# Optimization experiments

Measured on AMD Instinct MI355X. Metric: run time of the kernel, lower is better.

## Reference

```python
import jax, jax.numpy as jnp
import numpy as np

N_NODES = 131072
N_EDGES = 4194304
H1, H2 = 16, 1


def setup_inputs() -> dict:
    key = jax.random.key(0)
    k = jax.random.split(key, 6)
    x = jax.random.uniform(k[0], (N_NODES, 2), dtype=jnp.float32)
    edge_index = jax.random.randint(k[1], (2, N_EDGES), 0, N_NODES, dtype=jnp.int64)
    # GCNConv weights (glorot-ish scale) and zero biases
    W1 = jax.random.normal(k[2], (2, H1), dtype=jnp.float32) * 0.5
    b1 = jnp.zeros((H1,), dtype=jnp.float32)
    W2 = jax.random.normal(k[3], (H1, H2), dtype=jnp.float32) * 0.25
    b2 = jnp.zeros((H2,), dtype=jnp.float32)
    return {"x": x, "W1": W1, "b1": b1, "W2": W2, "b2": b2, "edge_index": edge_index}


def gcn_layer(x, W, b, src, dst, n):
    # PyG GCNConv: h = D^{-1/2} (A+I) D^{-1/2} (x W) + b  (self-loops already in src/dst)
    h = x @ W                                              # [N, F_out]
    deg = jax.ops.segment_sum(jnp.ones(dst.shape[0], h.dtype), dst, num_segments=n)
    dinv = jax.lax.rsqrt(deg)                              # deg >= 1 thanks to self-loops
    norm = dinv[src] * dinv[dst]                           # [E+N]
    out = jax.ops.segment_sum(h[src] * norm[:, None], dst, num_segments=n)
    return out + b


def reference(x, W1, b1, W2, b2, edge_index):
    n = x.shape[0]
    loops = jnp.arange(n, dtype=edge_index.dtype)
    src = jnp.concatenate([edge_index[0], loops])          # add self-loops once
    dst = jnp.concatenate([edge_index[1], loops])
    h = jax.nn.relu(gcn_layer(x, W1, b1, src, dst, n))
    h = gcn_layer(h, W2, b2, src, dst, n)                  # [N, 1]
    scores = jax.nn.sigmoid(h)
    return scores[edge_index[0]]                           # gather per-edge source score [E, 1]
```

## Files before the change

kernel.cpp:

```cpp
#include <hip/hip_runtime.h>
#include <cmath>

typedef unsigned int uint;

constexpr int N  = 131072;
constexpr int E  = 4194304;
constexpr int F  = 16;
constexpr int NB = 512;
constexpr int NBLK  = 512;
constexpr int SCT   = 512;
constexpr int GT    = 1024;
constexpr int CHUNK = 8192;
constexpr int EPT   = 16;
constexpr int CAPB  = 9216;
constexpr int LT    = 1024;
constexpr uint SENT = 0xFFFFFFFFu;

constexpr float S1 = 4194304.0f;
constexpr float S2 = 65536.0f;

__global__ void __launch_bounds__(SCT) k_scatter(
        const int* __restrict__ src, const int* __restrict__ dst,
        uint* __restrict__ part, uint* __restrict__ dirw) {
    __shared__ uint h[NB];
    __shared__ uint wsum[8];
    __shared__ uint vals[CHUNK];
    int t = threadIdx.x, g = blockIdx.x;
    int lane = t & 63, w = t >> 6;
    h[t] = 0;
    __syncthreads();
    int d[EPT], s[EPT];
    const int4* src4 = (const int4*)src;
    const int4* dst4 = (const int4*)dst;
    int base4 = g * (CHUNK / 4);
#pragma unroll
    for (int k = 0; k < EPT / 4; ++k) {
        int4 d4 = dst4[base4 + k * SCT + t];
        int4 s4 = src4[base4 + k * SCT + t];
        d[4 * k + 0] = d4.x; d[4 * k + 1] = d4.y; d[4 * k + 2] = d4.z; d[4 * k + 3] = d4.w;
        s[4 * k + 0] = s4.x; s[4 * k + 1] = s4.y; s[4 * k + 2] = s4.z; s[4 * k + 3] = s4.w;
        atomicAdd(&h[d4.x >> 8], 1u);
        atomicAdd(&h[d4.y >> 8], 1u);
        atomicAdd(&h[d4.z >> 8], 1u);
        atomicAdd(&h[d4.w >> 8], 1u);
    }
    __syncthreads();
    uint v = h[t];
    uint sv = v;
#pragma unroll
    for (int off = 1; off < 64; off <<= 1) {
        uint n = __shfl_up(sv, off);
        if (lane >= off) sv += n;
    }
    if (lane == 63) wsum[w] = sv;
    __syncthreads();
    uint wo = 0;
    for (int i = 0; i < w; ++i) wo += wsum[i];
    sv += wo;
    uint ex = sv - v;
    dirw[(size_t)g * NB + t] = v | (ex << 16);
    __syncthreads();
    h[t] = ex;
    __syncthreads();
#pragma unroll
    for (int k = 0; k < EPT; ++k) {
        int b = d[k] >> 8;
        uint slot = atomicAdd(&h[b], 1u);
        vals[slot] = ((uint)s[k] << 8) | (uint)(d[k] & 255);
    }
    __syncthreads();
    uint4* part4 = (uint4*)(part + (size_t)g * CHUNK);
    const uint4* vals4 = (const uint4*)vals;
#pragma unroll
    for (int k = 0; k < EPT / 4; ++k)
        part4[k * SCT + t] = vals4[k * SCT + t];
}

__global__ void __launch_bounds__(GT) k_gather(
        const uint* __restrict__ part, const uint* __restrict__ dirw,
        const float* __restrict__ x,
        uint* __restrict__ part2, uint* __restrict__ blen,
        float* __restrict__ dinv, float2* __restrict__ y) {
    __shared__ uint ps[NB + 1];
    __shared__ uint segoff[NB];
    __shared__ uint hw[16 * 256];
    __shared__ uint wsum[8];
    int t = threadIdx.x, b = blockIdx.x;
    int lane = t & 63, w = t >> 6;
#pragma unroll
    for (int k = 0; k < 4; ++k) hw[k * GT + t] = 0;
    if (t < NB) {
        uint pd = dirw[(size_t)t * NB + b];
        uint len = pd & 0xFFFFu;
        segoff[t] = (uint)t * CHUNK + (pd >> 16);
        uint sv = len;
#pragma unroll
        for (int off = 1; off < 64; off <<= 1) {
            uint n = __shfl_up(sv, off);
            if (lane >= off) sv += n;
        }
        if (lane == 63) wsum[w] = sv;
        ps[t] = sv - len;
    }
    __syncthreads();
    if (t < NB) {
        uint wo = 0;
        for (int i = 0; i < w; ++i) wo += wsum[i];
        ps[t] += wo;
    }
    if (t == 0) {
        uint Lt = 0;
#pragma unroll
        for (int i = 0; i < 8; ++i) Lt += wsum[i];
        ps[NB] = Lt;
    }
    __syncthreads();
    uint L = ps[NB];
    uint* o2 = part2 + (size_t)b * CAPB;
    int sub = lane >> 4, l16 = lane & 15;
#pragma unroll
    for (int pass = 0; pass < 8; ++pass) {
        int r = pass * 64 + w * 4 + sub;
        uint off = segoff[r], base = ps[r], len = ps[r + 1] - base;
        for (uint j = l16; j < len; j += 16) {
            uint pk = part[off + j];
            atomicAdd(&hw[w * 256 + (pk & 255u)], 1u);
            if (base + j < (uint)CAPB) o2[base + j] = pk;
        }
    }
    __syncthreads();
    uint Lc = (L > (uint)CAPB) ? (uint)CAPB : L;
    uint Lp = (Lc + 3u) & ~3u;
    uint i2 = Lc + (uint)t;
    if (i2 < Lp) o2[i2] = SENT;
    if (t == 0) blen[b] = Lp;
    if (t < 256) {
        uint c = 0;
#pragma unroll
        for (int k = 0; k < 16; ++k) c += hw[k * 256 + t];
        int node = (b << 8) + t;
        float di = rsqrtf(1.0f + (float)c);
        dinv[node] = di;
        float2 xv = ((const float2*)x)[node];
        y[node] = make_float2(di * xv.x, di * xv.y);
    }
}

__global__ void __launch_bounds__(LT) k_l1(
        const uint* __restrict__ part2, const uint* __restrict__ blen,
        const float2* __restrict__ y, const float* __restrict__ dinv,
        const float* __restrict__ W1, const float* __restrict__ b1,
        const float* __restrict__ W2, float* __restrict__ g2) {
    __shared__ int a0[16 * 256], a1[16 * 256];
    int t = threadIdx.x, b = blockIdx.x, w = t >> 6;
#pragma unroll
    for (int k = 0; k < 4; ++k) { a0[k * LT + t] = 0; a1[k * LT + t] = 0; }
    __syncthreads();
    uint L4 = blen[b] >> 2;
    const uint4* p4 = (const uint4*)(part2 + (size_t)b * CAPB);
    for (uint i = t; i < L4; i += LT) {
        uint4 q = p4[i];
        bool v0 = q.x != SENT, v1 = q.y != SENT, v2 = q.z != SENT, v3 = q.w != SENT;
        float2 y0, y1, y2, y3;
        if (v0) y0 = y[q.x >> 8];
        if (v1) y1 = y[q.y >> 8];
        if (v2) y2 = y[q.z >> 8];
        if (v3) y3 = y[q.w >> 8];
        if (v0) { atomicAdd(&a0[w * 256 + (q.x & 255u)], __float2int_rn(y0.x * S1));
                  atomicAdd(&a1[w * 256 + (q.x & 255u)], __float2int_rn(y0.y * S1)); }
        if (v1) { atomicAdd(&a0[w * 256 + (q.y & 255u)], __float2int_rn(y1.x * S1));
                  atomicAdd(&a1[w * 256 + (q.y & 255u)], __float2int_rn(y1.y * S1)); }
        if (v2) { atomicAdd(&a0[w * 256 + (q.z & 255u)], __float2int_rn(y2.x * S1));
                  atomicAdd(&a1[w * 256 + (q.z & 255u)], __float2int_rn(y2.y * S1)); }
        if (v3) { atomicAdd(&a0[w * 256 + (q.w & 255u)], __float2int_rn(y3.x * S1));
                  atomicAdd(&a1[w * 256 + (q.w & 255u)], __float2int_rn(y3.y * S1)); }
    }
    __syncthreads();
    if (t < 256) {
        int s0 = 0, s1 = 0;
#pragma unroll
        for (int k = 0; k < 16; ++k) { s0 += a0[k * 256 + t]; s1 += a1[k * 256 + t]; }
        int node = (b << 8) + t;
        float di = dinv[node];
        float2 yn = y[node];
        float A0 = di * ((float)s0 * (1.0f / S1) + yn.x);
        float A1 = di * ((float)s1 * (1.0f / S1) + yn.y);
        float acc = 0.0f;
#pragma unroll
        for (int f = 0; f < F; ++f) {
            float v = fmaf(A0, W1[f], fmaf(A1, W1[F + f], b1[f]));
            acc = fmaf(fmaxf(v, 0.0f), W2[f], acc);
        }
        g2[node] = di * acc;
    }
}

__global__ void __launch_bounds__(LT) k_l2(
        const uint* __restrict__ part2, const uint* __restrict__ blen,
        const float* __restrict__ g2, const float* __restrict__ dinv,
        const float* __restrict__ b2, float* __restrict__ scores) {
    __shared__ int a[16 * 256];
    int t = threadIdx.x, b = blockIdx.x, w = t >> 6;
#pragma unroll
    for (int k = 0; k < 4; ++k) a[k * LT + t] = 0;
    __syncthreads();
    uint L4 = blen[b] >> 2;
    const uint4* p4 = (const uint4*)(part2 + (size_t)b * CAPB);
    for (uint i = t; i < L4; i += LT) {
        uint4 q = p4[i];
        uint pk;
#pragma unroll
        for (int k = 0; k < 4; ++k) {
            pk = (k == 0) ? q.x : (k == 1) ? q.y : (k == 2) ? q.z : q.w;
            if (pk != SENT)
                atomicAdd(&a[w * 256 + (pk & 255u)], __float2int_rn(g2[pk >> 8] * S2));
        }
    }
    __syncthreads();
    if (t < 256) {
        int s = 0;
#pragma unroll
        for (int k = 0; k < 16; ++k) s += a[k * 256 + t];
        int node = (b << 8) + t;
        float acc = (float)s * (1.0f / S2);
        float v = fmaf(dinv[node], acc + g2[node], b2[0]);
        scores[node] = 1.0f / (1.0f + expf(-v));
    }
}

__global__ void k_out(const int* __restrict__ src, const float* __restrict__ scores,
                      float* __restrict__ out) {
    int i = blockIdx.x * blockDim.x + threadIdx.x;
    if (i >= E / 4) return;
    int4 s4 = ((const int4*)src)[i];
    float4 o;
    o.x = scores[s4.x];
    o.y = scores[s4.y];
    o.z = scores[s4.z];
    o.w = scores[s4.w];
    ((float4*)out)[i] = o;
}

extern "C" void kernel_launch(void* const* d_in, const int* in_sizes, int n_in,
                              void* d_out, int out_size, void* d_ws, size_t ws_size,
                              hipStream_t stream) {
    const float* x  = (const float*)d_in[0];
    const float* W1 = (const float*)d_in[1];
    const float* b1 = (const float*)d_in[2];
    const float* W2 = (const float*)d_in[3];
    const float* b2 = (const float*)d_in[4];
    const int*   ei = (const int*)d_in[5];
    const int* src = ei;
    const int* dst = ei + E;

    uint* dirw    = (uint*)d_ws;
    uint* blen    = dirw + (size_t)NBLK * NB;
    float* dinv   = (float*)(blen + NB);
    float2* y     = (float2*)(dinv + N);
    float* g2     = (float*)(y + N);
    float* scores = g2 + N;
    uint* part2   = (uint*)(scores + N);

    uint* part  = (uint*)d_out;
    float* out  = (float*)d_out;

    k_scatter<<<NBLK,        SCT, 0, stream>>>(src, dst, part, dirw);
    k_gather <<<NB,          GT,  0, stream>>>(part, dirw, x, part2, blen, dinv, y);
    k_l1     <<<NB,          LT,  0, stream>>>(part2, blen, y, dinv, W1, b1, W2, g2);
    k_l2     <<<NB,          LT,  0, stream>>>(part2, blen, g2, dinv, b2, scores);
    k_out    <<<E / 4 / 256, 256, 0, stream>>>(src, scores, out);
}
```

Baseline: 164.8 us.

## Fuse all stages into one persistent kernel with grid-wide barriers

Merges the scatter, gather, two aggregation layers and output gather into a single persistent kernel of 512 blocks. The stages are separated by software grid barriers built on global atomics. Each block keeps its destination-bucket edge list in shared memory (the old part2 staging buffer), along with its dinv, y and g2 values, which removes global round-trips and several launch overheads. The barrier requires all 512 blocks to be co-resident; if they are not, the timeout guard lets blocks run ahead and read incomplete data. Block size also drops from 1024 to 512 threads in the aggregation stages.

```diff
diff --git a/kernel.cpp b/kernel.cpp
--- a/kernel.cpp
+++ b/kernel.cpp
@@ -7,90 +7,123 @@
 constexpr int E  = 4194304;
 constexpr int F  = 16;
 constexpr int NB = 512;
-constexpr int NBLK  = 512;
-constexpr int SCT   = 512;
-constexpr int GT    = 1024;
+constexpr int T  = 512;
 constexpr int CHUNK = 8192;
 constexpr int EPT   = 16;
 constexpr int CAPB  = 9216;
-constexpr int LT    = 1024;
 constexpr uint SENT = 0xFFFFFFFFu;
 
 constexpr float S1 = 4194304.0f;
 constexpr float S2 = 65536.0f;
 
-__global__ void __launch_bounds__(SCT) k_scatter(
+__device__ __forceinline__ void gsync(uint* cnt, uint* rel, int t, uint gen) {
+    __syncthreads();
+    if (t == 0) {
+        __threadfence();
+        uint v = __hip_atomic_fetch_add(cnt, 1u, __ATOMIC_ACQ_REL,
+                                        __HIP_MEMORY_SCOPE_AGENT);
+        if (v == (uint)(NB - 1)) {
+            __hip_atomic_store(cnt, 0u, __ATOMIC_RELAXED, __HIP_MEMORY_SCOPE_AGENT);
+            __hip_atomic_store(rel, gen, __ATOMIC_RELEASE, __HIP_MEMORY_SCOPE_AGENT);
+        } else {
+            int guard = 0;
+            while (__hip_atomic_load(rel, __ATOMIC_ACQUIRE,
+                                     __HIP_MEMORY_SCOPE_AGENT) < gen) {
+                __builtin_amdgcn_s_sleep(2);
+                if (++guard > (1 << 22)) break;
+            }
+        }
+        __threadfence();
+    }
+    __syncthreads();
+}
+
+__global__ void k_init(uint* bar) {
+    if (threadIdx.x < 64) bar[threadIdx.x] = 0;
+}
+
+__global__ void __launch_bounds__(T, 4) k_fused(
         const int* __restrict__ src, const int* __restrict__ dst,
-        uint* __restrict__ part, uint* __restrict__ dirw) {
-    __shared__ uint h[NB];
+        const float* __restrict__ x,
+        const float* __restrict__ W1, const float* __restrict__ b1,
+        const float* __restrict__ W2, const float* __restrict__ b2,
+        uint* __restrict__ dirw, float2* __restrict__ y,
+        float* __restrict__ g2, float* __restrict__ scores,
+        uint* bar,
+        uint* part_out ) {
+    __shared__ uint stage[CAPB];
+    __shared__ uint ps[NB + 1];
+    __shared__ uint segoff[NB];
+    __shared__ int  bins0[8 * 256];
+    __shared__ int  bins1[8 * 256];
+    __shared__ float  dl[256];
+    __shared__ float2 yl[256];
+    __shared__ float  g2l[256];
     __shared__ uint wsum[8];
-    __shared__ uint vals[CHUNK];
+
     int t = threadIdx.x, g = blockIdx.x;
     int lane = t & 63, w = t >> 6;
-    h[t] = 0;
+    uint* part = part_out;
+    uint* cnt = bar;
+    uint* rel = bar + 32;
+
+    ps[t] = 0;
     __syncthreads();
     int d[EPT], s[EPT];
-    const int4* src4 = (const int4*)src;
-    const int4* dst4 = (const int4*)dst;
-    int base4 = g * (CHUNK / 4);
-#pragma unroll
-    for (int k = 0; k < EPT / 4; ++k) {
-        int4 d4 = dst4[base4 + k * SCT + t];
-        int4 s4 = src4[base4 + k * SCT + t];
-        d[4 * k + 0] = d4.x; d[4 * k + 1] = d4.y; d[4 * k + 2] = d4.z; d[4 * k + 3] = d4.w;
-        s[4 * k + 0] = s4.x; s[4 * k + 1] = s4.y; s[4 * k + 2] = s4.z; s[4 * k + 3] = s4.w;
-        atomicAdd(&h[d4.x >> 8], 1u);
-        atomicAdd(&h[d4.y >> 8], 1u);
-        atomicAdd(&h[d4.z >> 8], 1u);
-        atomicAdd(&h[d4.w >> 8], 1u);
-    }
-    __syncthreads();
-    uint v = h[t];
-    uint sv = v;
-#pragma unroll
-    for (int off = 1; off < 64; off <<= 1) {
-        uint n = __shfl_up(sv, off);
-        if (lane >= off) sv += n;
-    }
-    if (lane == 63) wsum[w] = sv;
-    __syncthreads();
-    uint wo = 0;
-    for (int i = 0; i < w; ++i) wo += wsum[i];
-    sv += wo;
-    uint ex = sv - v;
-    dirw[(size_t)g * NB + t] = v | (ex << 16);
-    __syncthreads();
-    h[t] = ex;
-    __syncthreads();
-#pragma unroll
-    for (int k = 0; k < EPT; ++k) {
-        int b = d[k] >> 8;
-        uint slot = atomicAdd(&h[b], 1u);
-        vals[slot] = ((uint)s[k] << 8) | (uint)(d[k] & 255);
-    }
-    __syncthreads();
-    uint4* part4 = (uint4*)(part + (size_t)g * CHUNK);
-    const uint4* vals4 = (const uint4*)vals;
-#pragma unroll
-    for (int k = 0; k < EPT / 4; ++k)
-        part4[k * SCT + t] = vals4[k * SCT + t];
-}
-
-__global__ void __launch_bounds__(GT) k_gather(
-        const uint* __restrict__ part, const uint* __restrict__ dirw,
-        const float* __restrict__ x,
-        uint* __restrict__ part2, uint* __restrict__ blen,
-        float* __restrict__ dinv, float2* __restrict__ y) {
-    __shared__ uint ps[NB + 1];
-    __shared__ uint segoff[NB];
-    __shared__ uint hw[16 * 256];
-    __shared__ uint wsum[8];
-    int t = threadIdx.x, b = blockIdx.x;
-    int lane = t & 63, w = t >> 6;
-#pragma unroll
-    for (int k = 0; k < 4; ++k) hw[k * GT + t] = 0;
-    if (t < NB) {
-        uint pd = dirw[(size_t)t * NB + b];
+    {
+        const int4* src4 = (const int4*)src;
+        const int4* dst4 = (const int4*)dst;
+        int base4 = g * (CHUNK / 4);
+#pragma unroll
+        for (int k = 0; k < EPT / 4; ++k) {
+            int4 d4 = dst4[base4 + k * T + t];
+            int4 s4 = src4[base4 + k * T + t];
+            d[4 * k + 0] = d4.x; d[4 * k + 1] = d4.y; d[4 * k + 2] = d4.z; d[4 * k + 3] = d4.w;
+            s[4 * k + 0] = s4.x; s[4 * k + 1] = s4.y; s[4 * k + 2] = s4.z; s[4 * k + 3] = s4.w;
+            atomicAdd(&ps[d4.x >> 8], 1u);
+            atomicAdd(&ps[d4.y >> 8], 1u);
+            atomicAdd(&ps[d4.z >> 8], 1u);
+            atomicAdd(&ps[d4.w >> 8], 1u);
+        }
+    }
+    __syncthreads();
+    {
+        uint v = ps[t];
+        uint sv = v;
+#pragma unroll
+        for (int off = 1; off < 64; off <<= 1) {
+            uint n = __shfl_up(sv, off);
+            if (lane >= off) sv += n;
+        }
+        if (lane == 63) wsum[w] = sv;
+        __syncthreads();
+        uint wo = 0;
+        for (int i = 0; i < w; ++i) wo += wsum[i];
+        sv += wo;
+        uint ex = sv - v;
+        dirw[(size_t)g * NB + t] = v | (ex << 16);
+        __syncthreads();
+        ps[t] = ex;
+        __syncthreads();
+#pragma unroll
+        for (int k = 0; k < EPT; ++k) {
+            int b = d[k] >> 8;
+            uint slot = atomicAdd(&ps[b], 1u);
+            stage[slot] = ((uint)s[k] << 8) | (uint)(d[k] & 255);
+        }
+        __syncthreads();
+        uint4* part4 = (uint4*)(part + (size_t)g * CHUNK);
+        const uint4* st4 = (const uint4*)stage;
+#pragma unroll
+        for (int k = 0; k < EPT / 4; ++k)
+            part4[k * T + t] = st4[k * T + t];
+    }
+    gsync(cnt, rel, t, 1);
+
+#pragma unroll
+    for (int k = 0; k < 4; ++k) bins0[k * T + t] = 0;
+    {
+        uint pd = dirw[(size_t)t * NB + g];
         uint len = pd & 0xFFFFu;
         segoff[t] = (uint)t * CHUNK + (pd >> 16);
         uint sv = len;
@@ -100,89 +133,84 @@
             if (lane >= off) sv += n;
         }
         if (lane == 63) wsum[w] = sv;
-        ps[t] = sv - len;
-    }
-    __syncthreads();
-    if (t < NB) {
+        uint part_ps = sv - len;
+        __syncthreads();
         uint wo = 0;
         for (int i = 0; i < w; ++i) wo += wsum[i];
-        ps[t] += wo;
-    }
-    if (t == 0) {
-        uint Lt = 0;
-#pragma unroll
-        for (int i = 0; i < 8; ++i) Lt += wsum[i];
-        ps[NB] = Lt;
-    }
-    __syncthreads();
-    uint L = ps[NB];
-    uint* o2 = part2 + (size_t)b * CAPB;
-    int sub = lane >> 4, l16 = lane & 15;
-#pragma unroll
-    for (int pass = 0; pass < 8; ++pass) {
-        int r = pass * 64 + w * 4 + sub;
-        uint off = segoff[r], base = ps[r], len = ps[r + 1] - base;
-        for (uint j = l16; j < len; j += 16) {
-            uint pk = part[off + j];
-            atomicAdd(&hw[w * 256 + (pk & 255u)], 1u);
-            if (base + j < (uint)CAPB) o2[base + j] = pk;
-        }
-    }
-    __syncthreads();
+        ps[t] = part_ps + wo;
+        if (t == 0) {
+            uint Lt = 0;
+#pragma unroll
+            for (int i = 0; i < 8; ++i) Lt += wsum[i];
+            ps[NB] = Lt;
+        }
+    }
+    __syncthreads();
+    uint L  = ps[NB];
     uint Lc = (L > (uint)CAPB) ? (uint)CAPB : L;
     uint Lp = (Lc + 3u) & ~3u;
-    uint i2 = Lc + (uint)t;
-    if (i2 < Lp) o2[i2] = SENT;
-    if (t == 0) blen[b] = Lp;
+    {
+        int sub = lane >> 4, l16 = lane & 15;
+#pragma unroll 2
+        for (int pass = 0; pass < 16; ++pass) {
+            int r = pass * 32 + w * 4 + sub;
+            uint off = segoff[r], base = ps[r], len = ps[r + 1] - base;
+            for (uint j = l16; j < len; j += 16) {
+                uint pk = part[off + j];
+                atomicAdd((uint*)&bins0[w * 256 + (pk & 255u)], 1u);
+                if (base + j < (uint)CAPB) stage[base + j] = pk;
+            }
+        }
+        uint i2 = Lc + (uint)t;
+        if (i2 < Lp) stage[i2] = SENT;
+    }
+    __syncthreads();
     if (t < 256) {
         uint c = 0;
 #pragma unroll
-        for (int k = 0; k < 16; ++k) c += hw[k * 256 + t];
-        int node = (b << 8) + t;
+        for (int k = 0; k < 8; ++k) c += (uint)bins0[k * 256 + t];
+        int node = (g << 8) + t;
         float di = rsqrtf(1.0f + (float)c);
-        dinv[node] = di;
+        dl[t] = di;
         float2 xv = ((const float2*)x)[node];
-        y[node] = make_float2(di * xv.x, di * xv.y);
-    }
-}
-
-__global__ void __launch_bounds__(LT) k_l1(
-        const uint* __restrict__ part2, const uint* __restrict__ blen,
-        const float2* __restrict__ y, const float* __restrict__ dinv,
-        const float* __restrict__ W1, const float* __restrict__ b1,
-        const float* __restrict__ W2, float* __restrict__ g2) {
-    __shared__ int a0[16 * 256], a1[16 * 256];
-    int t = threadIdx.x, b = blockIdx.x, w = t >> 6;
-#pragma unroll
-    for (int k = 0; k < 4; ++k) { a0[k * LT + t] = 0; a1[k * LT + t] = 0; }
-    __syncthreads();
-    uint L4 = blen[b] >> 2;
-    const uint4* p4 = (const uint4*)(part2 + (size_t)b * CAPB);
-    for (uint i = t; i < L4; i += LT) {
-        uint4 q = p4[i];
-        bool v0 = q.x != SENT, v1 = q.y != SENT, v2 = q.z != SENT, v3 = q.w != SENT;
-        float2 y0, y1, y2, y3;
-        if (v0) y0 = y[q.x >> 8];
-        if (v1) y1 = y[q.y >> 8];
-        if (v2) y2 = y[q.z >> 8];
-        if (v3) y3 = y[q.w >> 8];
-        if (v0) { atomicAdd(&a0[w * 256 + (q.x & 255u)], __float2int_rn(y0.x * S1));
-                  atomicAdd(&a1[w * 256 + (q.x & 255u)], __float2int_rn(y0.y * S1)); }
-        if (v1) { atomicAdd(&a0[w * 256 + (q.y & 255u)], __float2int_rn(y1.x * S1));
-                  atomicAdd(&a1[w * 256 + (q.y & 255u)], __float2int_rn(y1.y * S1)); }
-        if (v2) { atomicAdd(&a0[w * 256 + (q.z & 255u)], __float2int_rn(y2.x * S1));
-                  atomicAdd(&a1[w * 256 + (q.z & 255u)], __float2int_rn(y2.y * S1)); }
-        if (v3) { atomicAdd(&a0[w * 256 + (q.w & 255u)], __float2int_rn(y3.x * S1));
-                  atomicAdd(&a1[w * 256 + (q.w & 255u)], __float2int_rn(y3.y * S1)); }
+        float2 yv = make_float2(di * xv.x, di * xv.y);
+        yl[t] = yv;
+        y[node] = yv;
+    }
+    gsync(cnt, rel, t, 2);
+
+#pragma unroll
+    for (int k = 0; k < 4; ++k) { bins0[k * T + t] = 0; bins1[k * T + t] = 0; }
+    __syncthreads();
+    uint L4 = Lp >> 2;
+    {
+        const uint4* st4 = (const uint4*)stage;
+        for (uint i = t; i < L4; i += T) {
+            uint4 q = st4[i];
+            bool v0 = q.x != SENT, v1 = q.y != SENT, v2 = q.z != SENT, v3 = q.w != SENT;
+            float2 y0, y1, y2, y3;
+            if (v0) y0 = y[q.x >> 8];
+            if (v1) y1 = y[q.y >> 8];
+            if (v2) y2 = y[q.z >> 8];
+            if (v3) y3 = y[q.w >> 8];
+            if (v0) { atomicAdd(&bins0[w * 256 + (q.x & 255u)], __float2int_rn(y0.x * S1));
+                      atomicAdd(&bins1[w * 256 + (q.x & 255u)], __float2int_rn(y0.y * S1)); }
+            if (v1) { atomicAdd(&bins0[w * 256 + (q.y & 255u)], __float2int_rn(y1.x * S1));
+                      atomicAdd(&bins1[w * 256 + (q.y & 255u)], __float2int_rn(y1.y * S1)); }
+            if (v2) { atomicAdd(&bins0[w * 256 + (q.z & 255u)], __float2int_rn(y2.x * S1));
+                      atomicAdd(&bins1[w * 256 + (q.z & 255u)], __float2int_rn(y2.y * S1)); }
+            if (v3) { atomicAdd(&bins0[w * 256 + (q.w & 255u)], __float2int_rn(y3.x * S1));
+                      atomicAdd(&bins1[w * 256 + (q.w & 255u)], __float2int_rn(y3.y * S1)); }
+        }
     }
     __syncthreads();
     if (t < 256) {
         int s0 = 0, s1 = 0;
 #pragma unroll
-        for (int k = 0; k < 16; ++k) { s0 += a0[k * 256 + t]; s1 += a1[k * 256 + t]; }
-        int node = (b << 8) + t;
-        float di = dinv[node];
-        float2 yn = y[node];
+        for (int k = 0; k < 8; ++k) { s0 += bins0[k * 256 + t]; s1 += bins1[k * 256 + t]; }
+        int node = (g << 8) + t;
+        float di = dl[t];
+        float2 yn = yl[t];
         float A0 = di * ((float)s0 * (1.0f / S1) + yn.x);
         float A1 = di * ((float)s1 * (1.0f / S1) + yn.y);
         float acc = 0.0f;
@@ -191,54 +219,54 @@
             float v = fmaf(A0, W1[f], fmaf(A1, W1[F + f], b1[f]));
             acc = fmaf(fmaxf(v, 0.0f), W2[f], acc);
         }
-        g2[node] = di * acc;
-    }
-}
-
-__global__ void __launch_bounds__(LT) k_l2(
-        const uint* __restrict__ part2, const uint* __restrict__ blen,
-        const float* __restrict__ g2, const float* __restrict__ dinv,
-        const float* __restrict__ b2, float* __restrict__ scores) {
-    __shared__ int a[16 * 256];
-    int t = threadIdx.x, b = blockIdx.x, w = t >> 6;
-#pragma unroll
-    for (int k = 0; k < 4; ++k) a[k * LT + t] = 0;
-    __syncthreads();
-    uint L4 = blen[b] >> 2;
-    const uint4* p4 = (const uint4*)(part2 + (size_t)b * CAPB);
-    for (uint i = t; i < L4; i += LT) {
-        uint4 q = p4[i];
-        uint pk;
-#pragma unroll
-        for (int k = 0; k < 4; ++k) {
-            pk = (k == 0) ? q.x : (k == 1) ? q.y : (k == 2) ? q.z : q.w;
-            if (pk != SENT)
-                atomicAdd(&a[w * 256 + (pk & 255u)], __float2int_rn(g2[pk >> 8] * S2));
+        float gg = di * acc;
+        g2l[t] = gg;
+        g2[node] = gg;
+    }
+    gsync(cnt, rel, t, 3);
+
+#pragma unroll
+    for (int k = 0; k < 4; ++k) bins0[k * T + t] = 0;
+    __syncthreads();
+    {
+        uint L4b = Lp >> 2;
+        const uint4* st4 = (const uint4*)stage;
+        for (uint i = t; i < L4b; i += T) {
+            uint4 q = st4[i];
+            uint pk;
+#pragma unroll
+            for (int k = 0; k < 4; ++k) {
+                pk = (k == 0) ? q.x : (k == 1) ? q.y : (k == 2) ? q.z : q.w;
+                if (pk != SENT)
+                    atomicAdd(&bins0[w * 256 + (pk & 255u)], __float2int_rn(g2[pk >> 8] * S2));
+            }
         }
     }
     __syncthreads();
     if (t < 256) {
-        int s = 0;
-#pragma unroll
-        for (int k = 0; k < 16; ++k) s += a[k * 256 + t];
-        int node = (b << 8) + t;
-        float acc = (float)s * (1.0f / S2);
-        float v = fmaf(dinv[node], acc + g2[node], b2[0]);
+        int sacc = 0;
+#pragma unroll
+        for (int k = 0; k < 8; ++k) sacc += bins0[k * 256 + t];
+        int node = (g << 8) + t;
+        float acc = (float)sacc * (1.0f / S2);
+        float v = fmaf(dl[t], acc + g2l[t], b2[0]);
         scores[node] = 1.0f / (1.0f + expf(-v));
     }
-}
-
-__global__ void k_out(const int* __restrict__ src, const float* __restrict__ scores,
-                      float* __restrict__ out) {
-    int i = blockIdx.x * blockDim.x + threadIdx.x;
-    if (i >= E / 4) return;
-    int4 s4 = ((const int4*)src)[i];
-    float4 o;
-    o.x = scores[s4.x];
-    o.y = scores[s4.y];
-    o.z = scores[s4.z];
-    o.w = scores[s4.w];
-    ((float4*)out)[i] = o;
+    gsync(cnt, rel, t, 4);
+
+    {
+        const int4* s4p = (const int4*)src;
+        float4* o4 = (float4*)part_out;
+        for (int i = g * T + t; i < E / 4; i += NB * T) {
+            int4 s4 = s4p[i];
+            float4 o;
+            o.x = scores[s4.x];
+            o.y = scores[s4.y];
+            o.z = scores[s4.z];
+            o.w = scores[s4.w];
+            o4[i] = o;
+        }
+    }
 }
 
 extern "C" void kernel_launch(void* const* d_in, const int* in_sizes, int n_in,
@@ -253,20 +281,14 @@
     const int* src = ei;
     const int* dst = ei + E;
 
-    uint* dirw    = (uint*)d_ws;
-    uint* blen    = dirw + (size_t)NBLK * NB;
-    float* dinv   = (float*)(blen + NB);
-    float2* y     = (float2*)(dinv + N);
-    float* g2     = (float*)(y + N);
-    float* scores = g2 + N;
-    uint* part2   = (uint*)(scores + N);
-
-    uint* part  = (uint*)d_out;
-    float* out  = (float*)d_out;
-
-    k_scatter<<<NBLK,        SCT, 0, stream>>>(src, dst, part, dirw);
-    k_gather <<<NB,          GT,  0, stream>>>(part, dirw, x, part2, blen, dinv, y);
-    k_l1     <<<NB,          LT,  0, stream>>>(part2, blen, y, dinv, W1, b1, W2, g2);
-    k_l2     <<<NB,          LT,  0, stream>>>(part2, blen, g2, dinv, b2, scores);
-    k_out    <<<E / 4 / 256, 256, 0, stream>>>(src, scores, out);
-}
+    uint*   dirw   = (uint*)d_ws;
+    float2* y      = (float2*)(dirw + (size_t)NB * NB);
+    float*  g2     = (float*)(y + N);
+    float*  scores = g2 + N;
+    uint*   bar    = (uint*)(scores + N);
+    uint*   part_out = (uint*)d_out;
+
+    k_init <<<1, 64, 0, stream>>>(bar);
+    k_fused<<<NB, T, 0, stream>>>(src, dst, x, W1, b1, W2, b2,
+                                  dirw, y, g2, scores, bar, part_out);
+}
```

Measured after the change: 352.3 us. 114% more time.

## Scatter edges directly into per-bucket lists via global atomic offsets

Applied to the files above, without the earlier changes.

The scatter kernel now reserves space in each destination bucket with a global atomicAdd on per-bucket counters and writes its locally sorted edges straight into the final bucket lists. This removes the intermediate partition buffer and the separate gather pass that re-read and recopied it, leaving a lighter kernel that only counts degrees and pads the buckets. It also software-prefetches the next uint4 in the two aggregation loops. The trade-off is nondeterministic edge order within buckets, which adds float-to-int quantisation order effects, plus an extra init launch and scattered 16-lane global writes.

```diff
diff --git a/kernel.cpp b/kernel.cpp
--- a/kernel.cpp
+++ b/kernel.cpp
@@ -9,7 +9,6 @@
 constexpr int NB = 512;
 constexpr int NBLK  = 512;
 constexpr int SCT   = 512;
-constexpr int GT    = 1024;
 constexpr int CHUNK = 8192;
 constexpr int EPT   = 16;
 constexpr int CAPB  = 9216;
@@ -19,15 +18,20 @@
 constexpr float S1 = 4194304.0f;
 constexpr float S2 = 65536.0f;
 
+__global__ void k_init(uint* gcnt) {
+    gcnt[threadIdx.x] = 0;
+}
+
 __global__ void __launch_bounds__(SCT) k_scatter(
         const int* __restrict__ src, const int* __restrict__ dst,
-        uint* __restrict__ part, uint* __restrict__ dirw) {
-    __shared__ uint h[NB];
+        uint* __restrict__ gcnt, uint* __restrict__ part2) {
+    __shared__ uint ps[NB];
+    __shared__ uint gbase[NB];
+    __shared__ uint vals[CHUNK];
     __shared__ uint wsum[8];
-    __shared__ uint vals[CHUNK];
     int t = threadIdx.x, g = blockIdx.x;
     int lane = t & 63, w = t >> 6;
-    h[t] = 0;
+    ps[t] = 0;
     __syncthreads();
     int d[EPT], s[EPT];
     const int4* src4 = (const int4*)src;
@@ -39,13 +43,13 @@
         int4 s4 = src4[base4 + k * SCT + t];
         d[4 * k + 0] = d4.x; d[4 * k + 1] = d4.y; d[4 * k + 2] = d4.z; d[4 * k + 3] = d4.w;
         s[4 * k + 0] = s4.x; s[4 * k + 1] = s4.y; s[4 * k + 2] = s4.z; s[4 * k + 3] = s4.w;
-        atomicAdd(&h[d4.x >> 8], 1u);
-        atomicAdd(&h[d4.y >> 8], 1u);
-        atomicAdd(&h[d4.z >> 8], 1u);
-        atomicAdd(&h[d4.w >> 8], 1u);
-    }
-    __syncthreads();
-    uint v = h[t];
+        atomicAdd(&ps[d4.x >> 8], 1u);
+        atomicAdd(&ps[d4.y >> 8], 1u);
+        atomicAdd(&ps[d4.z >> 8], 1u);
+        atomicAdd(&ps[d4.w >> 8], 1u);
+    }
+    __syncthreads();
+    uint v = ps[t];
     uint sv = v;
 #pragma unroll
     for (int off = 1; off < 64; off <<= 1) {
@@ -53,91 +57,70 @@
         if (lane >= off) sv += n;
     }
     if (lane == 63) wsum[w] = sv;
+    gbase[t] = atomicAdd(&gcnt[t], v);
     __syncthreads();
     uint wo = 0;
     for (int i = 0; i < w; ++i) wo += wsum[i];
     sv += wo;
     uint ex = sv - v;
-    dirw[(size_t)g * NB + t] = v | (ex << 16);
-    __syncthreads();
-    h[t] = ex;
+    __syncthreads();
+    ps[t] = ex;
     __syncthreads();
 #pragma unroll
     for (int k = 0; k < EPT; ++k) {
         int b = d[k] >> 8;
-        uint slot = atomicAdd(&h[b], 1u);
+        uint slot = atomicAdd(&ps[b], 1u);
         vals[slot] = ((uint)s[k] << 8) | (uint)(d[k] & 255);
     }
     __syncthreads();
-    uint4* part4 = (uint4*)(part + (size_t)g * CHUNK);
-    const uint4* vals4 = (const uint4*)vals;
-#pragma unroll
-    for (int k = 0; k < EPT / 4; ++k)
-        part4[k * SCT + t] = vals4[k * SCT + t];
-}
-
-__global__ void __launch_bounds__(GT) k_gather(
-        const uint* __restrict__ part, const uint* __restrict__ dirw,
+    int sub = lane >> 4, l16 = lane & 15;
+#pragma unroll 2
+    for (int pass = 0; pass < 16; ++pass) {
+        int r = pass * 32 + w * 4 + sub;
+        uint end = ps[r];
+        uint beg = (r == 0) ? 0u : ps[r - 1];
+        uint len = end - beg;
+        uint gb = gbase[r];
+        uint* o = part2 + (size_t)r * CAPB;
+        for (uint j = l16; j < len; j += 16) {
+            uint gi = gb + j;
+            if (gi < (uint)CAPB) o[gi] = vals[beg + j];
+        }
+    }
+}
+
+__global__ void __launch_bounds__(LT) k_dy(
+        uint* __restrict__ part2, const uint* __restrict__ gcnt,
         const float* __restrict__ x,
-        uint* __restrict__ part2, uint* __restrict__ blen,
-        float* __restrict__ dinv, float2* __restrict__ y) {
-    __shared__ uint ps[NB + 1];
-    __shared__ uint segoff[NB];
-    __shared__ uint hw[16 * 256];
-    __shared__ uint wsum[8];
-    int t = threadIdx.x, b = blockIdx.x;
-    int lane = t & 63, w = t >> 6;
-#pragma unroll
-    for (int k = 0; k < 4; ++k) hw[k * GT + t] = 0;
-    if (t < NB) {
-        uint pd = dirw[(size_t)t * NB + b];
-        uint len = pd & 0xFFFFu;
-        segoff[t] = (uint)t * CHUNK + (pd >> 16);
-        uint sv = len;
-#pragma unroll
-        for (int off = 1; off < 64; off <<= 1) {
-            uint n = __shfl_up(sv, off);
-            if (lane >= off) sv += n;
-        }
-        if (lane == 63) wsum[w] = sv;
-        ps[t] = sv - len;
-    }
-    __syncthreads();
-    if (t < NB) {
-        uint wo = 0;
-        for (int i = 0; i < w; ++i) wo += wsum[i];
-        ps[t] += wo;
-    }
-    if (t == 0) {
-        uint Lt = 0;
-#pragma unroll
-        for (int i = 0; i < 8; ++i) Lt += wsum[i];
-        ps[NB] = Lt;
-    }
-    __syncthreads();
-    uint L = ps[NB];
-    uint* o2 = part2 + (size_t)b * CAPB;
-    int sub = lane >> 4, l16 = lane & 15;
-#pragma unroll
-    for (int pass = 0; pass < 8; ++pass) {
-        int r = pass * 64 + w * 4 + sub;
-        uint off = segoff[r], base = ps[r], len = ps[r + 1] - base;
-        for (uint j = l16; j < len; j += 16) {
-            uint pk = part[off + j];
-            atomicAdd(&hw[w * 256 + (pk & 255u)], 1u);
-            if (base + j < (uint)CAPB) o2[base + j] = pk;
-        }
-    }
-    __syncthreads();
+        uint* __restrict__ blen, float* __restrict__ dinv, float2* __restrict__ y) {
+    __shared__ uint cw[16 * 256];
+    int t = threadIdx.x, b = blockIdx.x, w = t >> 6;
+#pragma unroll
+    for (int k = 0; k < 4; ++k) cw[k * LT + t] = 0;
+    __syncthreads();
+    uint L  = gcnt[b];
     uint Lc = (L > (uint)CAPB) ? (uint)CAPB : L;
     uint Lp = (Lc + 3u) & ~3u;
+    uint* p = part2 + (size_t)b * CAPB;
+    uint L4 = Lc >> 2;
+    const uint4* p4 = (const uint4*)p;
+    for (uint i = t; i < L4; i += LT) {
+        uint4 q = p4[i];
+        atomicAdd(&cw[w * 256 + (q.x & 255u)], 1u);
+        atomicAdd(&cw[w * 256 + (q.y & 255u)], 1u);
+        atomicAdd(&cw[w * 256 + (q.z & 255u)], 1u);
+        atomicAdd(&cw[w * 256 + (q.w & 255u)], 1u);
+    }
+    uint it = (L4 << 2) + (uint)t;
+    if (it < Lc) atomicAdd(&cw[w * 256 + (p[it] & 255u)], 1u);
     uint i2 = Lc + (uint)t;
-    if (i2 < Lp) o2[i2] = SENT;
+    if (i2 < Lp) p[i2] = SENT;
     if (t == 0) blen[b] = Lp;
+    __syncthreads();
     if (t < 256) {
         uint c = 0;
 #pragma unroll
-        for (int k = 0; k < 16; ++k) c += hw[k * 256 + t];
+        for (int k = 0; k < 16; ++k) c += cw[k * 256 + t];
         int node = (b << 8) + t;
         float di = rsqrtf(1.0f + (float)c);
         dinv[node] = di;
@@ -158,8 +141,11 @@
     __syncthreads();
     uint L4 = blen[b] >> 2;
     const uint4* p4 = (const uint4*)(part2 + (size_t)b * CAPB);
-    for (uint i = t; i < L4; i += LT) {
-        uint4 q = p4[i];
+    uint i = t;
+    uint4 q = (i < L4) ? p4[i] : make_uint4(SENT, SENT, SENT, SENT);
+    while (i < L4) {
+        uint in = i + LT;
+        uint4 qn = (in < L4) ? p4[in] : make_uint4(SENT, SENT, SENT, SENT);
         bool v0 = q.x != SENT, v1 = q.y != SENT, v2 = q.z != SENT, v3 = q.w != SENT;
         float2 y0, y1, y2, y3;
         if (v0) y0 = y[q.x >> 8];
@@ -174,6 +160,7 @@
                   atomicAdd(&a1[w * 256 + (q.z & 255u)], __float2int_rn(y2.y * S1)); }
         if (v3) { atomicAdd(&a0[w * 256 + (q.w & 255u)], __float2int_rn(y3.x * S1));
                   atomicAdd(&a1[w * 256 + (q.w & 255u)], __float2int_rn(y3.y * S1)); }
+        q = qn; i = in;
     }
     __syncthreads();
     if (t < 256) {
@@ -206,15 +193,22 @@
     __syncthreads();
     uint L4 = blen[b] >> 2;
     const uint4* p4 = (const uint4*)(part2 + (size_t)b * CAPB);
-    for (uint i = t; i < L4; i += LT) {
-        uint4 q = p4[i];
-        uint pk;
-#pragma unroll
-        for (int k = 0; k < 4; ++k) {
-            pk = (k == 0) ? q.x : (k == 1) ? q.y : (k == 2) ? q.z : q.w;
-            if (pk != SENT)
-                atomicAdd(&a[w * 256 + (pk & 255u)], __float2int_rn(g2[pk >> 8] * S2));
-        }
+    uint i = t;
+    uint4 q = (i < L4) ? p4[i] : make_uint4(SENT, SENT, SENT, SENT);
+    while (i < L4) {
+        uint in = i + LT;
+        uint4 qn = (in < L4) ? p4[in] : make_uint4(SENT, SENT, SENT, SENT);
+        bool v0 = q.x != SENT, v1 = q.y != SENT, v2 = q.z != SENT, v3 = q.w != SENT;
+        float f0, f1, f2, f3;
+        if (v0) f0 = g2[q.x >> 8];
+        if (v1) f1 = g2[q.y >> 8];
+        if (v2) f2 = g2[q.z >> 8];
+        if (v3) f3 = g2[q.w >> 8];
+        if (v0) atomicAdd(&a[w * 256 + (q.x & 255u)], __float2int_rn(f0 * S2));
+        if (v1) atomicAdd(&a[w * 256 + (q.y & 255u)], __float2int_rn(f1 * S2));
+        if (v2) atomicAdd(&a[w * 256 + (q.z & 255u)], __float2int_rn(f2 * S2));
+        if (v3) atomicAdd(&a[w * 256 + (q.w & 255u)], __float2int_rn(f3 * S2));
+        q = qn; i = in;
     }
     __syncthreads();
     if (t < 256) {
@@ -253,20 +247,19 @@
     const int* src = ei;
     const int* dst = ei + E;
 
-    uint* dirw    = (uint*)d_ws;
-    uint* blen    = dirw + (size_t)NBLK * NB;
-    float* dinv   = (float*)(blen + NB);
-    float2* y     = (float2*)(dinv + N);
-    float* g2     = (float*)(y + N);
-    float* scores = g2 + N;
-    uint* part2   = (uint*)(scores + N);
-
-    uint* part  = (uint*)d_out;
-    float* out  = (float*)d_out;
-
-    k_scatter<<<NBLK,        SCT, 0, stream>>>(src, dst, part, dirw);
-    k_gather <<<NB,          GT,  0, stream>>>(part, dirw, x, part2, blen, dinv, y);
-    k_l1     <<<NB,          LT,  0, stream>>>(part2, blen, y, dinv, W1, b1, W2, g2);
-    k_l2     <<<NB,          LT,  0, stream>>>(part2, blen, g2, dinv, b2, scores);
-    k_out    <<<E / 4 / 256, 256, 0, stream>>>(src, scores, out);
-}
+    uint*   gcnt   = (uint*)d_ws;
+    uint*   blen   = gcnt + NB;
+    float*  dinv   = (float*)(blen + NB);
+    float2* y      = (float2*)(dinv + N);
+    float*  g2     = (float*)(y + N);
+    float*  scores = g2 + N;
+    uint*   part2  = (uint*)(scores + N);
+    float*  out    = (float*)d_out;
+
+    k_init   <<<1,             NB,  0, stream>>>(gcnt);
+    k_scatter<<<NBLK,          SCT, 0, stream>>>(src, dst, gcnt, part2);
+    k_dy     <<<NB,            LT,  0, stream>>>(part2, gcnt, x, blen, dinv, y);
+    k_l1     <<<NB,            LT,  0, stream>>>(part2, blen, y, dinv, W1, b1, W2, g2);
+    k_l2     <<<NB,            LT,  0, stream>>>(part2, blen, g2, dinv, b2, scores);
+    k_out    <<<E / 4 / 256,   256, 0, stream>>>(src, scores, out);
+}
```

Measured after the change: 169.2 us. +2.6%, slower.

## Pack two fixed-point feature sums into one 64-bit LDS atomic and prefetch edge loads

Applied to the files above, without the earlier changes.

Layer 1 now packs both feature channels into one 64-bit shared-memory atomic add. Each value gets a positive bias so the low half never borrows, and the bias is removed afterwards using the per-node degree, which the gather kernel now stores. This halves the number of LDS atomics in layer 1. Both aggregation loops also software-prefetch the next uint4 of packed edges, layer 2 issues its gathers before its atomics, and k_out handles eight edges per thread. The costs are an extra N-sized degree buffer, more registers, and the risk that a 32-bit half overflows on high-degree nodes.

```diff
diff --git a/kernel.cpp b/kernel.cpp
--- a/kernel.cpp
+++ b/kernel.cpp
@@ -2,6 +2,7 @@
 #include <cmath>
 
 typedef unsigned int uint;
+typedef unsigned long long ull;
 
 constexpr int N  = 131072;
 constexpr int E  = 4194304;
@@ -18,6 +19,7 @@
 
 constexpr float S1 = 4194304.0f;
 constexpr float S2 = 65536.0f;
+constexpr int  BIAS = 1 << 22;
 
 __global__ void __launch_bounds__(SCT) k_scatter(
         const int* __restrict__ src, const int* __restrict__ dst,
@@ -80,6 +82,7 @@
         const uint* __restrict__ part, const uint* __restrict__ dirw,
         const float* __restrict__ x,
         uint* __restrict__ part2, uint* __restrict__ blen,
+        uint* __restrict__ degg,
         float* __restrict__ dinv, float2* __restrict__ y) {
     __shared__ uint ps[NB + 1];
     __shared__ uint segoff[NB];
@@ -139,6 +142,7 @@
 #pragma unroll
         for (int k = 0; k < 16; ++k) c += hw[k * 256 + t];
         int node = (b << 8) + t;
+        degg[node] = c;
         float di = rsqrtf(1.0f + (float)c);
         dinv[node] = di;
         float2 xv = ((const float2*)x)[node];
@@ -149,38 +153,62 @@
 __global__ void __launch_bounds__(LT) k_l1(
         const uint* __restrict__ part2, const uint* __restrict__ blen,
         const float2* __restrict__ y, const float* __restrict__ dinv,
+        const uint* __restrict__ degg,
         const float* __restrict__ W1, const float* __restrict__ b1,
         const float* __restrict__ W2, float* __restrict__ g2) {
-    __shared__ int a0[16 * 256], a1[16 * 256];
+    __shared__ ull aa[16 * 256];
     int t = threadIdx.x, b = blockIdx.x, w = t >> 6;
 #pragma unroll
-    for (int k = 0; k < 4; ++k) { a0[k * LT + t] = 0; a1[k * LT + t] = 0; }
+    for (int k = 0; k < 4; ++k) aa[k * LT + t] = 0ull;
     __syncthreads();
     uint L4 = blen[b] >> 2;
     const uint4* p4 = (const uint4*)(part2 + (size_t)b * CAPB);
-    for (uint i = t; i < L4; i += LT) {
-        uint4 q = p4[i];
+    uint i = t;
+    uint4 q = (i < L4) ? p4[i] : make_uint4(SENT, SENT, SENT, SENT);
+    while (i < L4) {
+        uint in = i + LT;
+        uint4 qn = (in < L4) ? p4[in] : make_uint4(SENT, SENT, SENT, SENT);
         bool v0 = q.x != SENT, v1 = q.y != SENT, v2 = q.z != SENT, v3 = q.w != SENT;
         float2 y0, y1, y2, y3;
         if (v0) y0 = y[q.x >> 8];
         if (v1) y1 = y[q.y >> 8];
         if (v2) y2 = y[q.z >> 8];
         if (v3) y3 = y[q.w >> 8];
-        if (v0) { atomicAdd(&a0[w * 256 + (q.x & 255u)], __float2int_rn(y0.x * S1));
-                  atomicAdd(&a1[w * 256 + (q.x & 255u)], __float2int_rn(y0.y * S1)); }
-        if (v1) { atomicAdd(&a0[w * 256 + (q.y & 255u)], __float2int_rn(y1.x * S1));
-                  atomicAdd(&a1[w * 256 + (q.y & 255u)], __float2int_rn(y1.y * S1)); }
-        if (v2) { atomicAdd(&a0[w * 256 + (q.z & 255u)], __float2int_rn(y2.x * S1));
-                  atomicAdd(&a1[w * 256 + (q.z & 255u)], __float2int_rn(y2.y * S1)); }
-        if (v3) { atomicAdd(&a0[w * 256 + (q.w & 255u)], __float2int_rn(y3.x * S1));
-                  atomicAdd(&a1[w * 256 + (q.w & 255u)], __float2int_rn(y3.y * S1)); }
+        if (v0) {
+            uint i0 = (uint)(__float2int_rn(y0.x * S1) + BIAS);
+            uint i1 = (uint)(__float2int_rn(y0.y * S1) + BIAS);
+            atomicAdd(&aa[w * 256 + (q.x & 255u)], (ull)i0 | ((ull)i1 << 32));
+        }
+        if (v1) {
+            uint i0 = (uint)(__float2int_rn(y1.x * S1) + BIAS);
+            uint i1 = (uint)(__float2int_rn(y1.y * S1) + BIAS);
+            atomicAdd(&aa[w * 256 + (q.y & 255u)], (ull)i0 | ((ull)i1 << 32));
+        }
+        if (v2) {
+            uint i0 = (uint)(__float2int_rn(y2.x * S1) + BIAS);
+            uint i1 = (uint)(__float2int_rn(y2.y * S1) + BIAS);
+            atomicAdd(&aa[w * 256 + (q.z & 255u)], (ull)i0 | ((ull)i1 << 32));
+        }
+        if (v3) {
+            uint i0 = (uint)(__float2int_rn(y3.x * S1) + BIAS);
+            uint i1 = (uint)(__float2int_rn(y3.y * S1) + BIAS);
+            atomicAdd(&aa[w * 256 + (q.w & 255u)], (ull)i0 | ((ull)i1 << 32));
+        }
+        q = qn; i = in;
     }
     __syncthreads();
     if (t < 256) {
-        int s0 = 0, s1 = 0;
-#pragma unroll
-        for (int k = 0; k < 16; ++k) { s0 += a0[k * 256 + t]; s1 += a1[k * 256 + t]; }
+        uint s0b = 0, s1b = 0;
+#pragma unroll
+        for (int k = 0; k < 16; ++k) {
+            ull v = aa[k * 256 + t];
+            s0b += (uint)v;
+            s1b += (uint)(v >> 32);
+        }
         int node = (b << 8) + t;
+        uint deg = degg[node];
+        int s0 = (int)(s0b - deg * (uint)BIAS);
+        int s1 = (int)(s1b - deg * (uint)BIAS);
         float di = dinv[node];
         float2 yn = y[node];
         float A0 = di * ((float)s0 * (1.0f / S1) + yn.x);
@@ -206,15 +234,22 @@
     __syncthreads();
     uint L4 = blen[b] >> 2;
     const uint4* p4 = (const uint4*)(part2 + (size_t)b * CAPB);
-    for (uint i = t; i < L4; i += LT) {
-        uint4 q = p4[i];
-        uint pk;
-#pragma unroll
-        for (int k = 0; k < 4; ++k) {
-            pk = (k == 0) ? q.x : (k == 1) ? q.y : (k == 2) ? q.z : q.w;
-            if (pk != SENT)
-                atomicAdd(&a[w * 256 + (pk & 255u)], __float2int_rn(g2[pk >> 8] * S2));
-        }
+    uint i = t;
+    uint4 q = (i < L4) ? p4[i] : make_uint4(SENT, SENT, SENT, SENT);
+    while (i < L4) {
+        uint in = i + LT;
+        uint4 qn = (in < L4) ? p4[in] : make_uint4(SENT, SENT, SENT, SENT);
+        bool v0 = q.x != SENT, v1 = q.y != SENT, v2 = q.z != SENT, v3 = q.w != SENT;
+        float f0, f1, f2, f3;
+        if (v0) f0 = g2[q.x >> 8];
+        if (v1) f1 = g2[q.y >> 8];
+        if (v2) f2 = g2[q.z >> 8];
+        if (v3) f3 = g2[q.w >> 8];
+        if (v0) atomicAdd(&a[w * 256 + (q.x & 255u)], __float2int_rn(f0 * S2));
+        if (v1) atomicAdd(&a[w * 256 + (q.y & 255u)], __float2int_rn(f1 * S2));
+        if (v2) atomicAdd(&a[w * 256 + (q.z & 255u)], __float2int_rn(f2 * S2));
+        if (v3) atomicAdd(&a[w * 256 + (q.w & 255u)], __float2int_rn(f3 * S2));
+        q = qn; i = in;
     }
     __syncthreads();
     if (t < 256) {
@@ -231,14 +266,20 @@
 __global__ void k_out(const int* __restrict__ src, const float* __restrict__ scores,
                       float* __restrict__ out) {
     int i = blockIdx.x * blockDim.x + threadIdx.x;
-    if (i >= E / 4) return;
-    int4 s4 = ((const int4*)src)[i];
-    float4 o;
-    o.x = scores[s4.x];
-    o.y = scores[s4.y];
-    o.z = scores[s4.z];
-    o.w = scores[s4.w];
-    ((float4*)out)[i] = o;
+    if (i >= E / 8) return;
+    const int4* s4p = (const int4*)src;
+    int4 sa = s4p[2 * i], sb = s4p[2 * i + 1];
+    float4 oa, ob;
+    oa.x = scores[sa.x];
+    oa.y = scores[sa.y];
+    oa.z = scores[sa.z];
+    oa.w = scores[sa.w];
+    ob.x = scores[sb.x];
+    ob.y = scores[sb.y];
+    ob.z = scores[sb.z];
+    ob.w = scores[sb.w];
+    ((float4*)out)[2 * i]     = oa;
+    ((float4*)out)[2 * i + 1] = ob;
 }
 
 extern "C" void kernel_launch(void* const* d_in, const int* in_sizes, int n_in,
@@ -253,20 +294,23 @@
     const int* src = ei;
     const int* dst = ei + E;
 
-    uint* dirw    = (uint*)d_ws;
-    uint* blen    = dirw + (size_t)NBLK * NB;
-    float* dinv   = (float*)(blen + NB);
-    float2* y     = (float2*)(dinv + N);
-    float* g2     = (float*)(y + N);
-    float* scores = g2 + N;
-    uint* part2   = (uint*)(scores + N);
+    uint*   dirw   = (uint*)d_ws;
+    uint*   blen   = dirw + (size_t)NB * NB;
+    uint*   degg   = blen + NB;
+    float*  dinv   = (float*)(degg + N);
+    float2* y      = (float2*)(dinv + N);
+    float*  g2     = (float*)(y + N);
+    float*  scores = g2 + N;
+    uint*   part2  = (uint*)(scores + N);
 
     uint* part  = (uint*)d_out;
     float* out  = (float*)d_out;
 
     k_scatter<<<NBLK,        SCT, 0, stream>>>(src, dst, part, dirw);
-    k_gather <<<NB,          GT,  0, stream>>>(part, dirw, x, part2, blen, dinv, y);
-    k_l1     <<<NB,          LT,  0, stream>>>(part2, blen, y, dinv, W1, b1, W2, g2);
+    k_gather <<<NB,          GT,  0, stream>>>(part, dirw, x, part2, blen, degg,
+                                               dinv, y);
+    k_l1     <<<NB,          LT,  0, stream>>>(part2, blen, y, dinv, degg,
+                                               W1, b1, W2, g2);
     k_l2     <<<NB,          LT,  0, stream>>>(part2, blen, g2, dinv, b2, scores);
-    k_out    <<<E / 4 / 256, 256, 0, stream>>>(src, scores, out);
-}
+    k_out    <<<E / 8 / 256, 256, 0, stream>>>(src, scores, out);
+}
```

New measurement: 166.4 us. Within noise of the previous version (+0.9%).
